# Performance work log

Measured on AMD Instinct MI355X. Metric: run time of the kernel, lower is better.

Reference implementation:

```python
import jax, jax.numpy as jnp
import numpy as np

B, C, L = 16, 128, 2048


def setup_inputs() -> dict:
    key = jax.random.key(0)
    ks = jax.random.split(key, 7)
    s = 1.0 / np.sqrt(C)  # torch Conv1d default init scale
    x = jax.random.normal(ks[0], (B, C, L), dtype=jnp.float32)
    W1 = jax.random.uniform(ks[1], (C, C), jnp.float32, -s, s)
    b1 = jax.random.uniform(ks[2], (C,), jnp.float32, -s, s)
    W2 = jax.random.uniform(ks[3], (C, C), jnp.float32, -s, s)
    b2 = jax.random.uniform(ks[4], (C,), jnp.float32, -s, s)
    W3 = jax.random.uniform(ks[5], (C, C), jnp.float32, -s, s)
    b3 = jax.random.uniform(ks[6], (C,), jnp.float32, -s, s)
    return {"x": x, "W1": W1, "b1": b1, "W2": W2, "b2": b2, "W3": W3, "b3": b3}


def _conv1x1(x, W, b):
    # x: [B,C,L], W: [out,in] -> [B,out,L]
    return jnp.einsum('oc,bcl->bol', W, x) + b[None, :, None]


def reference(x, W1, b1, W2, b2, W3, b3):
    q = _conv1x1(x, W1, b1).transpose(0, 2, 1)  # [B,L,C]
    k = _conv1x1(x, W2, b2).transpose(0, 2, 1)  # [B,L,C]
    v = _conv1x1(x, W3, b3).transpose(0, 2, 1)  # [B,L,C]
    attn = jnp.einsum('bic,bjc->bij', q, k)     # [B,L,L]
    attn = jax.nn.softmax(attn, axis=-1)
    out = jnp.einsum('bij,bjc->bic', attn, v)   # [B,L,C]
    return out.transpose(0, 2, 1)               # [B,C,L]
```

## Files before the change

kernel.cpp:

```cpp
#include <hip/hip_runtime.h>
#include <hip/hip_bf16.h>
#include <stdint.h>

#define B_ 16
#define C_ 128
#define L_ 2048
#define LOG2E 1.4426950408889634f

typedef __attribute__((ext_vector_type(8))) short bf16x8;
typedef __attribute__((ext_vector_type(4))) float f32x4;
typedef __attribute__((ext_vector_type(16))) float f32x16;
typedef __attribute__((ext_vector_type(4))) unsigned int u32x4;

typedef __attribute__((address_space(3))) unsigned int lds_u32_t;
typedef const __attribute__((address_space(1))) unsigned int gbl_u32_t;

__device__ __forceinline__ void gload_lds16(const void* g, void* l) {
  __builtin_amdgcn_global_load_lds((gbl_u32_t*)g,
                                   (lds_u32_t*)(unsigned long long)l, 16, 0, 0);
}

__device__ __forceinline__ unsigned short f2bf(float x) {
  union { float f; unsigned u; } v; v.f = x;
  unsigned u = v.u;
  u += 0x7fffu + ((u >> 16) & 1u);
  return (unsigned short)(u >> 16);
}

__device__ __forceinline__ unsigned pk2(float a, float b) {
  return (unsigned)f2bf(a) | ((unsigned)f2bf(b) << 16);
}

__device__ __forceinline__ unsigned cvtpk_bf16(float lo, float hi_) {
  unsigned r;
  asm("v_cvt_pk_bf16_f32 %0, %1, %2" : "=v"(r) : "v"(lo), "v"(hi_));
  return r;
}

__device__ __forceinline__ float max3f(float a, float b, float c) {
  float r;
  asm("v_max3_f32 %0, %1, %2, %3" : "=v"(r) : "v"(a), "v"(b), "v"(c));
  return r;
}

__device__ __forceinline__ f32x16 z16() {
  f32x16 v;
#pragma unroll
  for (int i = 0; i < 16; ++i) v[i] = 0.f;
  return v;
}

__device__ __forceinline__ float tmax16(const f32x16& v) {
  float m0 = max3f(v[0], v[1], v[2]);
  float m1 = max3f(v[3], v[4], v[5]);
  float m2_ = max3f(v[6], v[7], v[8]);
  float m3 = max3f(v[9], v[10], v[11]);
  float m4 = max3f(v[12], v[13], v[14]);
  float a = max3f(m0, m1, m2_);
  float b = max3f(m3, m4, v[15]);
  return fmaxf(a, b);
}

__device__ __forceinline__ float tsum16(const f32x16& v) {
  float a0 = v[0] + v[1],  a1 = v[2] + v[3];
  float a2 = v[4] + v[5],  a3 = v[6] + v[7];
  float a4 = v[8] + v[9],  a5 = v[10] + v[11];
  float a6 = v[12] + v[13], a7 = v[14] + v[15];
  float b0 = a0 + a1, b1 = a2 + a3, b2 = a4 + a5, b3 = a6 + a7;
  return (b0 + b1) + (b2 + b3);
}

__global__ __launch_bounds__(256, 2) void proj_kernel(
    const float* __restrict__ x,
    const float* __restrict__ W1, const float* __restrict__ b1,
    const float* __restrict__ W2, const float* __restrict__ b2,
    const float* __restrict__ W3, const float* __restrict__ b3,
    unsigned short* __restrict__ Qo, unsigned short* __restrict__ Ko,
    unsigned short* __restrict__ Vt)
{
  __shared__ unsigned short Xt[64][136];
  __shared__ unsigned short Wl[128][136];

  const int b  = blockIdx.x & 15;
  const int lt = blockIdx.x >> 4;
  const int l0 = lt * 64;
  const int tid = threadIdx.x;
  const int w = tid >> 6, lane = tid & 63, li = lane & 15, lg = lane >> 4;

  for (int it = 0; it < 8; ++it) {
    int idx = tid + it * 256;
    int c = idx >> 4, f4 = idx & 15;
    const float4 vv = *(const float4*)(x + (size_t)(b * C_ + c) * L_ + l0 + f4 * 4);
    Xt[f4 * 4 + 0][c] = f2bf(vv.x);
    Xt[f4 * 4 + 1][c] = f2bf(vv.y);
    Xt[f4 * 4 + 2][c] = f2bf(vv.z);
    Xt[f4 * 4 + 3][c] = f2bf(vv.w);
  }

  auto stageW = [&](const float* W) {
    for (int it = 0; it < 16; ++it) {
      int idx = tid + it * 256;
      int o = idx >> 5, f4 = idx & 31;
      const float4 vv = *(const float4*)(W + (size_t)o * C_ + f4 * 4);
      unsigned short* p = &Wl[o][f4 * 4];
      p[0] = f2bf(vv.x); p[1] = f2bf(vv.y); p[2] = f2bf(vv.z); p[3] = f2bf(vv.w);
    }
  };

  auto computePhase = [&](const float* bias, unsigned short* Out, int mode, float sc) {
    f32x4 acc[8];
#pragma unroll
    for (int ni = 0; ni < 8; ++ni) acc[ni] = (f32x4){0.f, 0.f, 0.f, 0.f};
    bf16x8 af[4];
#pragma unroll
    for (int kk = 0; kk < 4; ++kk)
      af[kk] = *(const bf16x8*)&Xt[w * 16 + li][lg * 8 + kk * 32];
#pragma unroll
    for (int kk = 0; kk < 4; ++kk) {
#pragma unroll
      for (int ni = 0; ni < 8; ++ni) {
        bf16x8 bf = *(const bf16x8*)&Wl[ni * 16 + li][lg * 8 + kk * 32];
        acc[ni] = __builtin_amdgcn_mfma_f32_16x16x32_bf16(af[kk], bf, acc[ni], 0, 0, 0);
      }
    }
    if (mode == 0) {
#pragma unroll
      for (int ni = 0; ni < 8; ++ni) {
        float bv = bias[ni * 16 + li];
#pragma unroll
        for (int r = 0; r < 4; ++r) {
          int lrow = l0 + w * 16 + lg * 4 + r;
          Out[(size_t)(b * L_ + lrow) * C_ + ni * 16 + li] = f2bf((acc[ni][r] + bv) * sc);
        }
      }
    } else {
#pragma unroll
      for (int ni = 0; ni < 8; ++ni) {
        float bv = bias[ni * 16 + li];
        int o = ni * 16 + li;
        unsigned long long pw =
            (unsigned long long)pk2(acc[ni][0] + bv, acc[ni][1] + bv) |
            ((unsigned long long)pk2(acc[ni][2] + bv, acc[ni][3] + bv) << 32);
        *(unsigned long long*)(Out + (size_t)(b * C_ + o) * L_ + l0 + w * 16 + lg * 4) = pw;
      }
    }
  };

  stageW(W1);
  __syncthreads();
  computePhase(b1, Qo, 0, LOG2E);
  __syncthreads();
  stageW(W2);
  __syncthreads();
  computePhase(b2, Ko, 0, 1.0f);
  __syncthreads();
  stageW(W3);
  __syncthreads();
  computePhase(b3, Vt, 1, 1.0f);
}

__global__ __launch_bounds__(256, 2) void attn_kernel(
    const unsigned short* __restrict__ Q,
    const unsigned short* __restrict__ K,
    const unsigned short* __restrict__ Vt,
    float* __restrict__ out)
{
  __shared__ __align__(16) char smem[66560];

  const int b  = blockIdx.x & 15;
  const int qt = blockIdx.x >> 4;
  const int tid = threadIdx.x;
  const int w = tid >> 6, lane = tid & 63;
  const int q32 = lane & 31, hi = lane >> 5;
  const int qg = (w >> 1) & 1, jh = w & 1;
  const int qrow = qt * 64 + qg * 32 + q32;
  const size_t bLC = (size_t)b * L_ * C_;

  bf16x8 qf[8];
  {
    const unsigned short* qp = Q + bLC + (size_t)qrow * C_ + hi * 8;
#pragma unroll
    for (int kt = 0; kt < 8; ++kt) qf[kt] = *(const bf16x8*)(qp + kt * 16);
  }

  f32x16 oacc[4];
#pragma unroll
  for (int i = 0; i < 4; ++i) oacc[i] = z16();
  float m2 = -3e38f, lrun = 0.f;

  const int krow = jh * 32 + q32;
  int kvo[8];
#pragma unroll
  for (int kt = 0; kt < 8; ++kt)
    kvo[kt] = (krow << 8) + ((kt * 32 + hi * 16) ^ ((krow & 15) << 4));
  int vvo[8];
#pragma unroll
  for (int kj = 0; kj < 2; ++kj)
#pragma unroll
    for (int ct = 0; ct < 4; ++ct) {
      int rowc = ct * 32 + q32;
      vvo[kj * 4 + ct] = (rowc << 7) + (((jh * 2 + kj) * 32 + hi * 16) ^ ((rowc & 7) << 4));
    }

  int soff[8];
  const char* sp;
  int dbase, sadv;
  if (w < 2) {
    sp = (const char*)(K + bLC);
    dbase = w * 8192; sadv = 16384;
#pragma unroll
    for (int i2 = 0; i2 < 8; ++i2) {
      int d = w * 8192 + i2 * 1024 + lane * 16;
      int row = d >> 8, cb = d & 255;
      soff[i2] = row * 256 + (cb ^ ((row & 15) << 4));
    }
  } else {
    sp = (const char*)(Vt + bLC);
    dbase = 32768 + (w - 2) * 8192; sadv = 128;
#pragma unroll
    for (int i2 = 0; i2 < 8; ++i2) {
      int d = (w - 2) * 8192 + i2 * 1024 + lane * 16;
      int rc = d >> 7, cv = d & 127;
      soff[i2] = rc * 4096 + (cv ^ ((rc & 7) << 4));
    }
  }

  auto stage_next = [&](int curx) {
#pragma unroll
    for (int i2 = 0; i2 < 8; ++i2)
      gload_lds16(sp + soff[i2], &smem[dbase + (curx ^ 1) * 16384 + i2 * 1024]);
    sp += sadv;
  };

  auto body = [&](int cur, int vmN, int do_stage) {
    if (do_stage) stage_next(cur);
    __builtin_amdgcn_sched_barrier(0);
    if (vmN == 8) asm volatile("s_waitcnt vmcnt(8)" ::: "memory");
    else          asm volatile("s_waitcnt vmcnt(0)" ::: "memory");
    __builtin_amdgcn_s_barrier();
    __builtin_amdgcn_sched_barrier(0);

    const int KO = cur ? 16384 : 0;
    f32x16 s = z16();
    __builtin_amdgcn_s_setprio(1);
#pragma unroll
    for (int kt = 0; kt < 8; ++kt) {
      bf16x8 kf = *(const bf16x8*)&smem[KO + kvo[kt]];
      s = __builtin_amdgcn_mfma_f32_32x32x16_bf16(kf, qf[kt], s, 0, 0, 0);
    }
    __builtin_amdgcn_s_setprio(0);

    float pm = tmax16(s);
    pm = fmaxf(pm, __shfl_xor(pm, 32));
    if (!__all(pm - m2 <= 8.f)) {
      float mn = fmaxf(m2, pm);
      float al = exp2f(m2 - mn);
      lrun *= al;
#pragma unroll
      for (int ct = 0; ct < 4; ++ct) oacc[ct] = oacc[ct] * al;
      m2 = mn;
    }
#pragma unroll
    for (int r = 0; r < 16; ++r) s[r] = exp2f(s[r] - m2);
    float ps = tsum16(s);
    ps += __shfl_xor(ps, 32);
    lrun += ps;

    bf16x8 pf[2];
#pragma unroll
    for (int kj = 0; kj < 2; ++kj) {
      const int base = kj * 8;
      unsigned wl0 = cvtpk_bf16(s[base + 0], s[base + 1]);
      unsigned wl1 = cvtpk_bf16(s[base + 2], s[base + 3]);
      unsigned wh0 = cvtpk_bf16(s[base + 4], s[base + 5]);
      unsigned wh1 = cvtpk_bf16(s[base + 6], s[base + 7]);
      unsigned snd0 = hi ? wl0 : wh0;
      unsigned snd1 = hi ? wl1 : wh1;
      unsigned rcv0 = (unsigned)__shfl_xor((int)snd0, 32);
      unsigned rcv1 = (unsigned)__shfl_xor((int)snd1, 32);
      unsigned w0 = hi ? rcv0 : wl0;
      unsigned w1 = hi ? rcv1 : wl1;
      unsigned w2 = hi ? wh0 : rcv0;
      unsigned w3 = hi ? wh1 : rcv1;
      u32x4 pw = {w0, w1, w2, w3};
      pf[kj] = *reinterpret_cast<bf16x8*>(&pw);
    }

    const int VO = 32768 + KO;
    __builtin_amdgcn_s_setprio(1);
#pragma unroll
    for (int kj = 0; kj < 2; ++kj)
#pragma unroll
      for (int ct = 0; ct < 4; ++ct) {
        bf16x8 vf = *(const bf16x8*)&smem[VO + vvo[kj * 4 + ct]];
        oacc[ct] = __builtin_amdgcn_mfma_f32_32x32x16_bf16(vf, pf[kj], oacc[ct], 0, 0, 0);
      }
    __builtin_amdgcn_s_setprio(0);

    __builtin_amdgcn_sched_barrier(0);
    asm volatile("s_waitcnt lgkmcnt(0)" ::: "memory");
    __builtin_amdgcn_s_barrier();
    __builtin_amdgcn_sched_barrier(0);
  };

  stage_next(1);
  __builtin_amdgcn_sched_barrier(0);

  for (int tt = 0; tt < 15; ++tt) {
    body(0, 8, 1);
    body(1, 8, 1);
  }
  body(0, 8, 1);
  body(1, 0, 0);

  float* mlb = (float*)(smem + 65536);
  if (hi == 0) {
    mlb[(w * 32 + q32) * 2 + 0] = m2;
    mlb[(w * 32 + q32) * 2 + 1] = lrun;
  }
  __syncthreads();
  const float mB = mlb[((w ^ 1) * 32 + q32) * 2 + 0];
  const float lB = mlb[((w ^ 1) * 32 + q32) * 2 + 1];
  const float mstar = fmaxf(m2, mB);
  const float aown  = exp2f(m2 - mstar);
  float* scrb = (float*)smem + (size_t)(qg * 64 + lane) * 33;
  float* ob = out + (size_t)b * C_ * L_ + qrow;
  float inv = 0.f;
  if (jh == 0) {
    const float aB = exp2f(mB - mstar);
    inv = 1.0f / (lrun * aown + lB * aB);
  }
  __syncthreads();
  if (jh == 1) {
#pragma unroll
    for (int r = 0; r < 16; ++r) {
      scrb[r]      = oacc[0][r] * aown;
      scrb[16 + r] = oacc[1][r] * aown;
    }
  }
  __syncthreads();
  if (jh == 0) {
#pragma unroll
    for (int ct = 0; ct < 2; ++ct)
#pragma unroll
      for (int r = 0; r < 16; ++r) {
        float v = oacc[ct][r] * aown + scrb[ct * 16 + r];
        int c = ct * 32 + (r & 3) + 8 * (r >> 2) + 4 * hi;
        ob[(size_t)c * L_] = v * inv;
      }
  }
  __syncthreads();
  if (jh == 1) {
#pragma unroll
    for (int r = 0; r < 16; ++r) {
      scrb[r]      = oacc[2][r] * aown;
      scrb[16 + r] = oacc[3][r] * aown;
    }
  }
  __syncthreads();
  if (jh == 0) {
#pragma unroll
    for (int ct = 0; ct < 2; ++ct)
#pragma unroll
      for (int r = 0; r < 16; ++r) {
        float v = oacc[2 + ct][r] * aown + scrb[ct * 16 + r];
        int c = (2 + ct) * 32 + (r & 3) + 8 * (r >> 2) + 4 * hi;
        ob[(size_t)c * L_] = v * inv;
      }
  }
}

extern "C" void kernel_launch(void* const* d_in, const int* in_sizes, int n_in,
                              void* d_out, int out_size, void* d_ws, size_t ws_size,
                              hipStream_t stream) {
  (void)in_sizes; (void)n_in; (void)out_size; (void)ws_size;
  const float* x  = (const float*)d_in[0];
  const float* W1 = (const float*)d_in[1];
  const float* b1 = (const float*)d_in[2];
  const float* W2 = (const float*)d_in[3];
  const float* b2 = (const float*)d_in[4];
  const float* W3 = (const float*)d_in[5];
  const float* b3 = (const float*)d_in[6];

  unsigned short* Q  = (unsigned short*)d_ws;
  unsigned short* K  = Q + (size_t)B_ * L_ * C_;
  unsigned short* Vt = K + (size_t)B_ * L_ * C_;

  proj_kernel<<<512, 256, 0, stream>>>(x, W1, b1, W2, b2, W3, b3, Q, K, Vt);
  attn_kernel<<<512, 256, 0, stream>>>(Q, K, Vt, (float*)d_out);
}
```

Baseline: 75.92 us.

## Software-pipeline QK of next tile with softmax and PV of current tile

Restructures the flash-attention inner loop so the QK^T MFMAs for the next K tile are issued before the softmax and PV of the previous tile. K and V staging are split, with V loads issued after the barrier, so each buffer is refilled on its own schedule. This lets independent MFMA work overlap the exp/shuffle softmax phase. It costs a second live score accumulator (more VGPRs) and makes the prologue and epilogue wait and barrier logic more intricate.

```diff
diff --git a/kernel.cpp b/kernel.cpp
--- a/kernel.cpp
+++ b/kernel.cpp
@@ -225,22 +225,24 @@
     }
   }
 
-  auto stage_next = [&](int curx) {
-#pragma unroll
-    for (int i2 = 0; i2 < 8; ++i2)
-      gload_lds16(sp + soff[i2], &smem[dbase + (curx ^ 1) * 16384 + i2 * 1024]);
-    sp += sadv;
-  };
-
-  auto body = [&](int cur, int vmN, int do_stage) {
-    if (do_stage) stage_next(cur);
-    __builtin_amdgcn_sched_barrier(0);
-    if (vmN == 8) asm volatile("s_waitcnt vmcnt(8)" ::: "memory");
-    else          asm volatile("s_waitcnt vmcnt(0)" ::: "memory");
-    __builtin_amdgcn_s_barrier();
-    __builtin_amdgcn_sched_barrier(0);
-
-    const int KO = cur ? 16384 : 0;
+  auto stageK = [&](int dest) {
+    if (w < 2) {
+#pragma unroll
+      for (int i2 = 0; i2 < 8; ++i2)
+        gload_lds16(sp + soff[i2], &smem[dbase + dest * 16384 + i2 * 1024]);
+      sp += sadv;
+    }
+  };
+  auto stageV = [&](int dest) {
+    if (w >= 2) {
+#pragma unroll
+      for (int i2 = 0; i2 < 8; ++i2)
+        gload_lds16(sp + soff[i2], &smem[dbase + dest * 16384 + i2 * 1024]);
+      sp += sadv;
+    }
+  };
+
+  auto QK = [&](int KO, f32x16& sD) {
     f32x16 s = z16();
     __builtin_amdgcn_s_setprio(1);
 #pragma unroll
@@ -249,7 +251,10 @@
       s = __builtin_amdgcn_mfma_f32_32x32x16_bf16(kf, qf[kt], s, 0, 0, 0);
     }
     __builtin_amdgcn_s_setprio(0);
-
+    sD = s;
+  };
+
+  auto SM_PV = [&](f32x16& s, int VO) {
     float pm = tmax16(s);
     pm = fmaxf(pm, __shfl_xor(pm, 32));
     if (!__all(pm - m2 <= 8.f)) {
@@ -286,7 +291,6 @@
       pf[kj] = *reinterpret_cast<bf16x8*>(&pw);
     }
 
-    const int VO = 32768 + KO;
     __builtin_amdgcn_s_setprio(1);
 #pragma unroll
     for (int kj = 0; kj < 2; ++kj)
@@ -296,22 +300,47 @@
         oacc[ct] = __builtin_amdgcn_mfma_f32_32x32x16_bf16(vf, pf[kj], oacc[ct], 0, 0, 0);
       }
     __builtin_amdgcn_s_setprio(0);
-
+  };
+
+  f32x16 sA, sB;
+
+  stageK(0);
+  stageV(0);
+  stageK(1);
+  __builtin_amdgcn_sched_barrier(0);
+  asm volatile("s_waitcnt vmcnt(8)" ::: "memory");
+  __builtin_amdgcn_s_barrier();
+  __builtin_amdgcn_sched_barrier(0);
+  QK(0, sA);
+  __builtin_amdgcn_sched_barrier(0);
+  asm volatile("s_waitcnt lgkmcnt(0)" ::: "memory");
+  __builtin_amdgcn_s_barrier();
+  __builtin_amdgcn_sched_barrier(0);
+  stageV(1);
+
+  auto iter = [&](int par, int doStage, int vm0) {
+    if (doStage) stageK(1 - par);
+    __builtin_amdgcn_sched_barrier(0);
+    if (vm0) asm volatile("s_waitcnt vmcnt(0)" ::: "memory");
+    else     asm volatile("s_waitcnt vmcnt(8)" ::: "memory");
+    __builtin_amdgcn_s_barrier();
+    __builtin_amdgcn_sched_barrier(0);
+    if (par) { QK(16384, sB); SM_PV(sA, 32768); }
+    else     { QK(0, sA);     SM_PV(sB, 32768 + 16384); }
     __builtin_amdgcn_sched_barrier(0);
     asm volatile("s_waitcnt lgkmcnt(0)" ::: "memory");
     __builtin_amdgcn_s_barrier();
     __builtin_amdgcn_sched_barrier(0);
-  };
-
-  stage_next(1);
-  __builtin_amdgcn_sched_barrier(0);
+    if (doStage) stageV(1 - par);
+  };
 
   for (int tt = 0; tt < 15; ++tt) {
-    body(0, 8, 1);
-    body(1, 8, 1);
-  }
-  body(0, 8, 1);
-  body(1, 0, 0);
+    iter(1, 1, 0);
+    iter(0, 1, 0);
+  }
+  iter(1, 0, 1);
+
+  SM_PV(sB, 32768 + 16384);
 
   float* mlb = (float*)(smem + 65536);
   if (hi == 0) {
```

Result: no change. 75.40 us (-0.7%).

## Drop K/V double buffering to halve LDS and raise occupancy

Applied to the files above, without the earlier changes.

Replaces the double-buffered K/V LDS pipeline, which issued async prefetch with vmcnt waits, with a single buffer that is loaded and then synchronised with __syncthreads each tile. LDS use is halved and launch bounds request 4 blocks per CU instead of 2. The aim is to hide memory latency through more resident waves rather than software pipelining. In exchange each tile now exposes its full global-load latency inside the block, and it takes two barriers per iteration.

```diff
diff --git a/kernel.cpp b/kernel.cpp
--- a/kernel.cpp
+++ b/kernel.cpp
@@ -159,13 +159,13 @@
   computePhase(b3, Vt, 1, 1.0f);
 }
 
-__global__ __launch_bounds__(256, 2) void attn_kernel(
+__global__ __launch_bounds__(256, 4) void attn_kernel(
     const unsigned short* __restrict__ Q,
     const unsigned short* __restrict__ K,
     const unsigned short* __restrict__ Vt,
     float* __restrict__ out)
 {
-  __shared__ __align__(16) char smem[66560];
+  __shared__ __align__(16) char smem[33792];
 
   const int b  = blockIdx.x & 15;
   const int qt = blockIdx.x >> 4;
@@ -199,7 +199,8 @@
 #pragma unroll
     for (int ct = 0; ct < 4; ++ct) {
       int rowc = ct * 32 + q32;
-      vvo[kj * 4 + ct] = (rowc << 7) + (((jh * 2 + kj) * 32 + hi * 16) ^ ((rowc & 7) << 4));
+      vvo[kj * 4 + ct] = 16384 + (rowc << 7) +
+                         (((jh * 2 + kj) * 32 + hi * 16) ^ ((rowc & 7) << 4));
     }
 
   int soff[8];
@@ -216,7 +217,7 @@
     }
   } else {
     sp = (const char*)(Vt + bLC);
-    dbase = 32768 + (w - 2) * 8192; sadv = 128;
+    dbase = 16384 + (w - 2) * 8192; sadv = 128;
 #pragma unroll
     for (int i2 = 0; i2 < 8; ++i2) {
       int d = (w - 2) * 8192 + i2 * 1024 + lane * 16;
@@ -225,27 +226,18 @@
     }
   }
 
-  auto stage_next = [&](int curx) {
+  for (int t = 0; t < 32; ++t) {
 #pragma unroll
     for (int i2 = 0; i2 < 8; ++i2)
-      gload_lds16(sp + soff[i2], &smem[dbase + (curx ^ 1) * 16384 + i2 * 1024]);
+      gload_lds16(sp + soff[i2], &smem[dbase + i2 * 1024]);
     sp += sadv;
-  };
-
-  auto body = [&](int cur, int vmN, int do_stage) {
-    if (do_stage) stage_next(cur);
-    __builtin_amdgcn_sched_barrier(0);
-    if (vmN == 8) asm volatile("s_waitcnt vmcnt(8)" ::: "memory");
-    else          asm volatile("s_waitcnt vmcnt(0)" ::: "memory");
-    __builtin_amdgcn_s_barrier();
-    __builtin_amdgcn_sched_barrier(0);
-
-    const int KO = cur ? 16384 : 0;
+    __syncthreads();
+
     f32x16 s = z16();
     __builtin_amdgcn_s_setprio(1);
 #pragma unroll
     for (int kt = 0; kt < 8; ++kt) {
-      bf16x8 kf = *(const bf16x8*)&smem[KO + kvo[kt]];
+      bf16x8 kf = *(const bf16x8*)&smem[kvo[kt]];
       s = __builtin_amdgcn_mfma_f32_32x32x16_bf16(kf, qf[kt], s, 0, 0, 0);
     }
     __builtin_amdgcn_s_setprio(0);
@@ -286,34 +278,20 @@
       pf[kj] = *reinterpret_cast<bf16x8*>(&pw);
     }
 
-    const int VO = 32768 + KO;
     __builtin_amdgcn_s_setprio(1);
 #pragma unroll
     for (int kj = 0; kj < 2; ++kj)
 #pragma unroll
       for (int ct = 0; ct < 4; ++ct) {
-        bf16x8 vf = *(const bf16x8*)&smem[VO + vvo[kj * 4 + ct]];
+        bf16x8 vf = *(const bf16x8*)&smem[vvo[kj * 4 + ct]];
         oacc[ct] = __builtin_amdgcn_mfma_f32_32x32x16_bf16(vf, pf[kj], oacc[ct], 0, 0, 0);
       }
     __builtin_amdgcn_s_setprio(0);
 
-    __builtin_amdgcn_sched_barrier(0);
-    asm volatile("s_waitcnt lgkmcnt(0)" ::: "memory");
-    __builtin_amdgcn_s_barrier();
-    __builtin_amdgcn_sched_barrier(0);
-  };
-
-  stage_next(1);
-  __builtin_amdgcn_sched_barrier(0);
-
-  for (int tt = 0; tt < 15; ++tt) {
-    body(0, 8, 1);
-    body(1, 8, 1);
-  }
-  body(0, 8, 1);
-  body(1, 0, 0);
-
-  float* mlb = (float*)(smem + 65536);
+    __syncthreads();
+  }
+
+  float* mlb = (float*)(smem + 32768);
   if (hi == 0) {
     mlb[(w * 32 + q32) * 2 + 0] = m2;
     mlb[(w * 32 + q32) * 2 + 1] = lrun;
```

After: 126.9 us. +67.1%, slower.
